# Performance work log

Hardware: AMD Instinct MI355X
Metric: run time of the kernel (lower is better)

The kernel has to match this reference:

```python
import jax, jax.numpy as jnp
import numpy as np
from math import factorial

LS = (0, 1, 2)
N_NODES = 30000
N_EDGES = 480000
E_CH = 2
C_IN = 4


def _cg_coeff(j1, m1, j2, m2, j, m):
    if m != m1 + m2 or j < abs(j1 - j2) or j > j1 + j2:
        return 0.0
    f = factorial
    pre = ((2 * j + 1) * f(j + j1 - j2) * f(j - j1 + j2) * f(j1 + j2 - j) / f(j1 + j2 + j + 1)) ** 0.5
    pre *= (f(j + m) * f(j - m) * f(j1 - m1) * f(j1 + m1) * f(j2 - m2) * f(j2 + m2)) ** 0.5
    s = 0.0
    for k in range(0, j1 + j2 - j + 1):
        d = [k, j1 + j2 - j - k, j1 - m1 - k, j2 + m2 - k, j - j2 + m1 + k, j - j1 - m2 + k]
        if any(v < 0 for v in d):
            continue
        s += (-1) ** k / np.prod([float(f(v)) for v in d])
    return pre * s


def _cg_matrix(l1, l2, l):
    # [2l+1, 2l1+1, 2l2+1]
    M = np.zeros((2 * l + 1, 2 * l1 + 1, 2 * l2 + 1), dtype=np.float32)
    for m in range(-l, l + 1):
        for m1 in range(-l1, l1 + 1):
            for m2 in range(-l2, l2 + 1):
                M[m + l, m1 + l1, m2 + l2] = _cg_coeff(l1, m1, l2, m2, l, m)
    return jnp.asarray(M)

CG_MATS = {}
for _l1 in LS:
    for _l2 in LS:
        for _lo in LS:
            if abs(_l1 - _l2) <= _lo <= _l1 + _l2:
                CG_MATS[(_l1, _l2, _lo)] = _cg_matrix(_l1, _l2, _lo)


def mp_layer(xs, edge_vals, src, dst, n_nodes):
    # gather src features, outer-product with edge channels, scatter-add to dst
    out = {}
    for l, x in xs.items():
        msg = x[src][:, None, :, :] * edge_vals[:, :, None, None]  # [E, Ech, C, 2l+1]
        msg = msg.reshape(msg.shape[0], -1, 2 * l + 1)
        out[l] = jax.ops.segment_sum(msg, dst, num_segments=n_nodes)
    return out


def cg_product(a, b):
    out = {}
    for lo in LS:
        chunks = []
        for l1 in LS:
            for l2 in LS:
                if abs(l1 - l2) <= lo <= l1 + l2:
                    C = CG_MATS[(l1, l2, lo)]
                    t = jnp.einsum('mpq,ncp,ndq->ncdm', C, a[l1], b[l2])
                    chunks.append(t.reshape(t.shape[0], -1, 2 * lo + 1))
        out[lo] = jnp.concatenate(chunks, axis=1)
    return out


def so3_linear(parts, weights):
    return {l: jnp.einsum('ncm,co->nom', parts[l], weights[l]) for l in parts}


def setup_inputs() -> dict:
    key = jax.random.key(0)
    ks = jax.random.split(key, 16)
    inp = {}
    for i, l in enumerate(LS):
        inp[f'x{l}'] = jax.random.normal(ks[i], (N_NODES, C_IN, 2 * l + 1), dtype=jnp.float32)
    inp['edge_vals'] = jax.random.normal(ks[3], (N_EDGES, E_CH), dtype=jnp.float32)
    w_shapes = {'W_xx0': (48, 8), 'W_xx1': (96, 8), 'W_xx2': (96, 8),
                'W_yx0': (96, 8), 'W_yx1': (192, 8), 'W_yx2': (192, 8),
                'W_yy0': (192, 8), 'W_yy1': (384, 8), 'W_yy2': (384, 8)}
    for i, (name, shp) in enumerate(w_shapes.items()):
        inp[name] = jax.random.normal(ks[4 + i], shp, dtype=jnp.float32) * 0.05
    inp['edge_idx'] = jax.random.randint(ks[13], (2, N_EDGES), 0, N_NODES, dtype=jnp.int64)
    return inp


def reference(x0, x1, x2, edge_vals,
              W_xx0, W_xx1, W_xx2,
              W_yx0, W_yx1, W_yx2,
              W_yy0, W_yy1, W_yy2,
              edge_idx):
    xs = {0: x0, 1: x1, 2: x2}
    src, dst = edge_idx[0], edge_idx[1]
    n = x0.shape[0]
    W_xx = {0: W_xx0, 1: W_xx1, 2: W_xx2}
    W_yx = {0: W_yx0, 1: W_yx1, 2: W_yx2}
    W_yy = {0: W_yy0, 1: W_yy1, 2: W_yy2}
    y = mp_layer(xs, edge_vals, src, dst, n)
    y_mp_mp = so3_linear(cg_product(y, y), W_yy)
    y_mp_id = so3_linear(cg_product(y, xs), W_yx)
    y_id_id = so3_linear(cg_product(xs, xs), W_xx)
    return tuple(y_mp_mp[l] + y_mp_id[l] + y_id_id[l] for l in LS)
```

## Files before the change

kernel.cpp:

```cpp
#include <hip/hip_runtime.h>
#include <stdint.h>

#define NN 30000
#define NE 480000
#define NB 469

constexpr double cfact(int n){ double r=1.0; for(int i=2;i<=n;i++) r*=(double)i; return r; }
constexpr double csqrt_(double x){ if(x<=0.0) return 0.0; double g = x<1.0?1.0:x; for(int i=0;i<200;i++) g = 0.5*(g + x/g); return g; }
constexpr double cg_coeff(int j1,int m1,int j2,int m2,int j,int m){
  if(m != m1+m2) return 0.0;
  int dj = j1-j2; if(dj<0) dj=-dj;
  if(j < dj || j > j1+j2) return 0.0;
  double pre = csqrt_((2*j+1)*cfact(j+j1-j2)*cfact(j-j1+j2)*cfact(j1+j2-j)/cfact(j1+j2+j+1));
  pre = pre * csqrt_(cfact(j+m)*cfact(j-m)*cfact(j1-m1)*cfact(j1+m1)*cfact(j2-m2)*cfact(j2+m2));
  double s = 0.0;
  for(int k=0;k<=j1+j2-j;k++){
    int d0=k, d1=j1+j2-j-k, d2=j1-m1-k, d3=j2+m2-k, d4=j-j2+m1+k, d5=j-j1-m2+k;
    if(d0<0||d1<0||d2<0||d3<0||d4<0||d5<0) continue;
    double term = 1.0/(cfact(d0)*cfact(d1)*cfact(d2)*cfact(d3)*cfact(d4)*cfact(d5));
    s += (k&1) ? -term : term;
  }
  return pre*s;
}

template<int L1,int L2,int LO> struct CGTab { float v[2*LO+1][2*L1+1][2*L2+1]; };

template<int L1,int L2,int LO>
constexpr CGTab<L1,L2,LO> make_cg(){
  CGTab<L1,L2,LO> t{};
  for(int m=-LO;m<=LO;m++)
    for(int p=-L1;p<=L1;p++)
      for(int q=-L2;q<=L2;q++)
        t.v[m+LO][p+L1][q+L2] = (float)cg_coeff(L1,p,L2,q,LO,m);
  return t;
}
template<int L1,int L2,int LO>
constexpr CGTab<L1,L2,LO> CG_TAB = make_cg<L1,L2,LO>();

template<int L1,int L2,int LO>
__device__ __forceinline__ void build_T(const float* av, const float* bv, float* T){
  constexpr int MA=2*L1+1, MB=2*L2+1, MO=2*LO+1;
  #pragma unroll
  for(int m=0;m<MO;m++) T[m]=0.f;
  #pragma unroll
  for(int m=0;m<MO;m++)
    #pragma unroll
    for(int p=0;p<MA;p++)
      #pragma unroll
      for(int q=0;q<MB;q++){
        const float cg = CG_TAB<L1,L2,LO>.v[m][p][q];
        if(cg!=0.0f) T[m]=fmaf(cg*av[p],bv[q],T[m]);
      }
}

template<int L1,int L2,int LO,int CA,int CB>
__device__ __forceinline__ void do_chunk(const float* __restrict__ A,
                                         const float* __restrict__ B,
                                         const float* __restrict__ W, int wb,
                                         float acc[8][2*LO+1])
{
  constexpr int MA=2*L1+1, MB=2*L2+1, MO=2*LO+1;
  float bv[CB][MB];
  #pragma unroll
  for(int d=0;d<CB;d++)
    #pragma unroll
    for(int q=0;q<MB;q++) bv[d][q] = B[(d*MB+q)*64];
  #pragma unroll 1
  for(int c=0;c<CA;c++){
    float av[MA];
    #pragma unroll
    for(int p=0;p<MA;p++) av[p] = A[(c*MA+p)*64];
    #pragma unroll
    for(int d=0;d<CB;d++){
      float T[MO];
      build_T<L1,L2,LO>(av, bv[d], T);
      const float* wr = W + (wb + c*CB + d)*8;
      #pragma unroll
      for(int o=0;o<8;o++){
        float w = wr[o];
        #pragma unroll
        for(int m=0;m<MO;m++) acc[o][m] = fmaf(w, T[m], acc[o][m]);
      }
    }
  }
}

template<int L1,int L2,int LO,int C,int SGN>
__device__ __forceinline__ void do_chunk_fold(const float* __restrict__ A1,
    const float* __restrict__ A2, const float* __restrict__ W, int wb1, int wb2,
    float acc[8][2*LO+1])
{
  constexpr int MA=2*L1+1, MB=2*L2+1, MO=2*LO+1;
  float bv[C][MB];
  #pragma unroll
  for(int d=0;d<C;d++)
    #pragma unroll
    for(int q=0;q<MB;q++) bv[d][q] = A2[(d*MB+q)*64];
  #pragma unroll 1
  for(int c=0;c<C;c++){
    float av[MA];
    #pragma unroll
    for(int p=0;p<MA;p++) av[p] = A1[(c*MA+p)*64];
    #pragma unroll
    for(int d=0;d<C;d++){
      float T[MO];
      build_T<L1,L2,LO>(av, bv[d], T);
      const float* w1 = W + (wb1 + c*C + d)*8;
      const float* w2 = W + (wb2 + d*C + c)*8;
      #pragma unroll
      for(int o=0;o<8;o++){
        float wf = (SGN>0) ? (w1[o] + w2[o]) : (w1[o] - w2[o]);
        #pragma unroll
        for(int m=0;m<MO;m++) acc[o][m] = fmaf(wf, T[m], acc[o][m]);
      }
    }
  }
}

template<int L,int LO,int C,int SGN>
__device__ __forceinline__ void do_chunk_tri(const float* __restrict__ Al,
    const float* __restrict__ W, int wb, float acc[8][2*LO+1])
{
  constexpr int M=2*L+1, MO=2*LO+1;
  float bv[C][M];
  #pragma unroll
  for(int d=0;d<C;d++)
    #pragma unroll
    for(int q=0;q<M;q++) bv[d][q] = Al[(d*M+q)*64];
  #pragma unroll 1
  for(int c=0;c<C-1;c++){
    float av[M];
    #pragma unroll
    for(int p=0;p<M;p++) av[p] = Al[(c*M+p)*64];
    #pragma unroll
    for(int d=0;d<C;d++){
      if(d > c){
        float T[MO];
        build_T<L,L,LO>(av, bv[d], T);
        const float* w1 = W + (wb + c*C + d)*8;
        const float* w2 = W + (wb + d*C + c)*8;
        #pragma unroll
        for(int o=0;o<8;o++){
          float wf = (SGN>0) ? (w1[o] + w2[o]) : (w1[o] - w2[o]);
          #pragma unroll
          for(int m=0;m<MO;m++) acc[o][m] = fmaf(wf, T[m], acc[o][m]);
        }
      }
    }
  }
}

template<int L,int LO,int C>
__device__ __forceinline__ void do_chunk_diagO(const float* __restrict__ Al,
    const float* __restrict__ W, int wb, float acc[8][2*LO+1])
{
  constexpr int M=2*L+1, MO=2*LO+1;
  #pragma unroll 1
  for(int c=0;c<C;c++){
    float av[M];
    #pragma unroll
    for(int p=0;p<M;p++) av[p] = Al[(c*M+p)*64];
    float T[MO];
    build_T<L,L,LO>(av, av, T);
    const float* wr = W + (wb + c*C + c)*8;
    #pragma unroll
    for(int o=0;o<8;o++){
      float w = wr[o];
      #pragma unroll
      for(int m=0;m<MO;m++) acc[o][m] = fmaf(w, T[m], acc[o][m]);
    }
  }
}

template<int LO,int CA,int CB>
__device__ __forceinline__ void run_chunks(
    const float* a0,const float* a1,const float* a2,
    const float* b0,const float* b1,const float* b2,
    const float* __restrict__ W, float acc[8][2*LO+1])
{
  constexpr int S = CA*CB;
  if constexpr (LO==0){
    do_chunk<0,0,0,CA,CB>(a0,b0,W,0*S,acc);
    do_chunk<1,1,0,CA,CB>(a1,b1,W,1*S,acc);
    do_chunk<2,2,0,CA,CB>(a2,b2,W,2*S,acc);
  } else if constexpr (LO==1){
    do_chunk<0,1,1,CA,CB>(a0,b1,W,0*S,acc);
    do_chunk<1,0,1,CA,CB>(a1,b0,W,1*S,acc);
    do_chunk<1,1,1,CA,CB>(a1,b1,W,2*S,acc);
    do_chunk<1,2,1,CA,CB>(a1,b2,W,3*S,acc);
    do_chunk<2,1,1,CA,CB>(a2,b1,W,4*S,acc);
    do_chunk<2,2,1,CA,CB>(a2,b2,W,5*S,acc);
  } else {
    do_chunk<0,2,2,CA,CB>(a0,b2,W,0*S,acc);
    do_chunk<1,1,2,CA,CB>(a1,b1,W,1*S,acc);
    do_chunk<1,2,2,CA,CB>(a1,b2,W,2*S,acc);
    do_chunk<2,0,2,CA,CB>(a2,b0,W,3*S,acc);
    do_chunk<2,1,2,CA,CB>(a2,b1,W,4*S,acc);
    do_chunk<2,2,2,CA,CB>(a2,b2,W,5*S,acc);
  }
}

template<int LO,int C>
__device__ __forceinline__ void run_chunks_sym(
    const float* a0,const float* a1,const float* a2,
    const float* __restrict__ W, float acc[8][2*LO+1])
{
  constexpr int S = C*C;
  if constexpr (LO==0){
    do_chunk_tri<0,0,C,+1>(a0,W,0*S,acc);  do_chunk_diagO<0,0,C>(a0,W,0*S,acc);
    do_chunk_tri<1,0,C,+1>(a1,W,1*S,acc);  do_chunk_diagO<1,0,C>(a1,W,1*S,acc);
    do_chunk_tri<2,0,C,+1>(a2,W,2*S,acc);  do_chunk_diagO<2,0,C>(a2,W,2*S,acc);
  } else if constexpr (LO==1){
    do_chunk_fold<0,1,1,C,+1>(a0,a1,W,0*S,1*S,acc);
    do_chunk_tri <1,1,C,-1>(a1,W,2*S,acc);
    do_chunk_fold<1,2,1,C,+1>(a1,a2,W,3*S,4*S,acc);
    do_chunk_tri <2,1,C,-1>(a2,W,5*S,acc);
  } else {
    do_chunk_fold<0,2,2,C,+1>(a0,a2,W,0*S,3*S,acc);
    do_chunk_tri <1,2,C,+1>(a1,W,1*S,acc);  do_chunk_diagO<1,2,C>(a1,W,1*S,acc);
    do_chunk_fold<1,2,2,C,-1>(a1,a2,W,2*S,4*S,acc);
    do_chunk_tri <2,2,C,+1>(a2,W,5*S,acc);  do_chunk_diagO<2,2,C>(a2,W,5*S,acc);
  }
}

template<int PROD,int LO>
__device__ __forceinline__ void do_item_lds(int lane,
    const float* __restrict__ sx, const float* __restrict__ sy,
    const float* __restrict__ W, float* __restrict__ so)
{
  const float *y0 = sy + lane, *y1 = sy + 8*64 + lane, *y2 = sy + 32*64 + lane;
  const float *x0 = sx + lane, *x1 = sx + 4*64 + lane, *x2 = sx + 16*64 + lane;
  constexpr int MO = 2*LO+1;

  float acc[8][MO];
  #pragma unroll
  for(int o=0;o<8;o++)
    #pragma unroll
    for(int m=0;m<MO;m++) acc[o][m]=0.f;

  if constexpr (PROD==0)      run_chunks_sym<LO,8>(y0,y1,y2,W,acc);
  else if constexpr (PROD==2) run_chunks_sym<LO,4>(x0,x1,x2,W,acc);
  else                        run_chunks<LO,8,4>(y0,y1,y2,x0,x1,x2,W,acc);

  constexpr int OB = (LO==0)?0:((LO==1)?8:32);
  #pragma unroll
  for(int o=0;o<8;o++)
    #pragma unroll
    for(int m=0;m<MO;m++)
      atomicAdd(&so[(OB + o*MO + m)*65 + lane], acc[o][m]);
}

struct WPtrs {
  const float* xx[3];
  const float* yx[3];
  const float* yy[3];
};

__global__ __launch_bounds__(256,2) void fused_kernel(
    const float* __restrict__ x0, const float* __restrict__ x1, const float* __restrict__ x2,
    const float4* __restrict__ edges, const int* __restrict__ offs,
    WPtrs w, float* __restrict__ out)
{
  __shared__ float sy[72*64];
  __shared__ float sx[36*64];
  __shared__ float so[72*65];

  const int tid = threadIdx.x;
  const int node0 = blockIdx.x*64;

  #pragma unroll
  for(int i=tid;i<72*65;i+=256) so[i]=0.f;

  for(int i=tid;i<64*4;i+=256){
    int gi = node0*4 + i;
    sx[(i&3)*64 + (i>>2)] = (gi < NN*4) ? x0[gi] : 0.f;
  }
  for(int i=tid;i<64*12;i+=256){
    int gi = node0*12 + i;
    sx[(4 + i%12)*64 + i/12] = (gi < NN*12) ? x1[gi] : 0.f;
  }
  for(int i=tid;i<64*20;i+=256){
    int gi = node0*20 + i;
    sx[(16 + i%20)*64 + i/20] = (gi < NN*20) ? x2[gi] : 0.f;
  }

  {
    int ln = tid >> 2, c = tid & 3;
    int gn = node0 + ln;
    float a0[2]={0.f,0.f};
    float a1[2][3]={}, a2[2][5]={};
    if(gn < NN){
      int k0 = offs[gn], k1 = offs[gn+1];
      for(int k=k0;k<k1;k++){
        float4 ed = edges[k];
        int src = __float_as_int(ed.x);
        float e0 = ed.y, e1 = ed.z;
        float v0 = x0[src*4 + c];
        const float* q1 = x1 + src*12 + c*3;
        const float* q2 = x2 + src*20 + c*5;
        a0[0] = fmaf(e0, v0, a0[0]);
        a0[1] = fmaf(e1, v0, a0[1]);
        #pragma unroll
        for(int m=0;m<3;m++){ float v=q1[m]; a1[0][m]=fmaf(e0,v,a1[0][m]); a1[1][m]=fmaf(e1,v,a1[1][m]); }
        #pragma unroll
        for(int m=0;m<5;m++){ float v=q2[m]; a2[0][m]=fmaf(e0,v,a2[0][m]); a2[1][m]=fmaf(e1,v,a2[1][m]); }
      }
    }
    #pragma unroll
    for(int ech=0;ech<2;ech++){
      int ch = ech*4 + c;
      sy[ch*64 + ln] = a0[ech];
      #pragma unroll
      for(int m=0;m<3;m++) sy[(8  + ch*3 + m)*64 + ln] = a1[ech][m];
      #pragma unroll
      for(int m=0;m<5;m++) sy[(32 + ch*5 + m)*64 + ln] = a2[ech][m];
    }
  }
  __syncthreads();

  {
    int lane = tid & 63, slot = tid >> 6;
    switch(slot){
      case 0: do_item_lds<1,2>(lane,sx,sy,w.yx[2],so); break;
      case 1: do_item_lds<0,2>(lane,sx,sy,w.yy[2],so); break;
      case 2: do_item_lds<0,1>(lane,sx,sy,w.yy[1],so);
              do_item_lds<2,2>(lane,sx,sy,w.xx[2],so);
              do_item_lds<0,0>(lane,sx,sy,w.yy[0],so); break;
      case 3: do_item_lds<1,1>(lane,sx,sy,w.yx[1],so);
              do_item_lds<2,1>(lane,sx,sy,w.xx[1],so);
              do_item_lds<1,0>(lane,sx,sy,w.yx[0],so);
              do_item_lds<2,0>(lane,sx,sy,w.xx[0],so); break;
    }
  }
  __syncthreads();

  for(int i=tid;i<64*8;i+=256){
    int n=i>>3, o=i&7;
    if(node0+n < NN) out[(node0+n)*8 + o] = so[o*65 + n];
  }
  for(int i=tid;i<64*24;i+=256){
    int n=i/24, r=i-n*24;
    if(node0+n < NN) out[NN*8 + (node0+n)*24 + r] = so[(8+r)*65 + n];
  }
  for(int i=tid;i<64*40;i+=256){
    int n=i/40, r=i-n*40;
    if(node0+n < NN) out[NN*32 + (node0+n)*40 + r] = so[(32+r)*65 + n];
  }
}

__global__ __launch_bounds__(256) void hist_kernel(const int* __restrict__ idx, int* __restrict__ cnt)
{
  int e = blockIdx.x*256 + threadIdx.x;
  if(e >= NE) return;
  atomicAdd(&cnt[idx[NE + e]], 1);
}

__global__ __launch_bounds__(256) void scan1_kernel(const int* __restrict__ cnt,
    int* __restrict__ offs, int* __restrict__ bt)
{
  __shared__ int wsum[4], wexc[4];
  int b = blockIdx.x, tid = threadIdx.x;
  int lane = tid & 63, wid = tid >> 6;
  int i0 = b*512 + tid*2;
  int v0 = (i0   < NN) ? cnt[i0]   : 0;
  int v1 = (i0+1 < NN) ? cnt[i0+1] : 0;
  int v = v0+v1, s = v;
  #pragma unroll
  for(int o=1;o<64;o<<=1){ int t=__shfl_up(s,o,64); if(lane>=o) s+=t; }
  if(lane==63) wsum[wid]=s;
  __syncthreads();
  if(tid<4){
    int wv=wsum[tid], x=wv;
    #pragma unroll
    for(int o=1;o<4;o<<=1){ int t=__shfl_up(x,o,4); if(tid>=o) x+=t; }
    wexc[tid]=x-wv;
    if(tid==3) bt[b]=x;
  }
  __syncthreads();
  int excl = s - v + wexc[wid];
  if(i0   < NN) offs[i0]   = excl;
  if(i0+1 < NN) offs[i0+1] = excl + v0;
}

__global__ __launch_bounds__(64) void scan2_kernel(int* __restrict__ bt,
    int* __restrict__ bte, int* __restrict__ offs)
{
  int tid = threadIdx.x;
  int v = bt[tid], s = v;
  #pragma unroll
  for(int o=1;o<64;o<<=1){ int t=__shfl_up(s,o,64); if(tid>=o) s+=t; }
  bte[tid] = s - v;
  if(tid==63) offs[NN] = s;
}

__global__ __launch_bounds__(512) void scan3_kernel(int* __restrict__ offs,
    const int* __restrict__ bte, int* __restrict__ cur)
{
  int i = blockIdx.x*512 + threadIdx.x;
  if(i >= NN) return;
  int o = offs[i] + bte[blockIdx.x];
  offs[i] = o;
  cur[i]  = o;
}

__global__ __launch_bounds__(256) void scatter_kernel(const int* __restrict__ idx,
    const float* __restrict__ ev, int* __restrict__ cur, float4* __restrict__ edges)
{
  int e = blockIdx.x*256 + threadIdx.x;
  if(e >= NE) return;
  int dst = idx[NE + e];
  int pos = atomicAdd(&cur[dst], 1);
  float4 r;
  r.x = __int_as_float(idx[e]);
  r.y = ev[2*e];
  r.z = ev[2*e+1];
  r.w = 0.f;
  edges[pos] = r;
}

extern "C" void kernel_launch(void* const* d_in, const int* in_sizes, int n_in,
                              void* d_out, int out_size, void* d_ws, size_t ws_size,
                              hipStream_t stream)
{
  const float* x0 = (const float*)d_in[0];
  const float* x1 = (const float*)d_in[1];
  const float* x2 = (const float*)d_in[2];
  const float* ev = (const float*)d_in[3];
  const int* idx  = (const int*)d_in[13];

  WPtrs w;
  for(int l=0;l<3;l++){
    w.xx[l] = (const float*)d_in[4+l];
    w.yx[l] = (const float*)d_in[7+l];
    w.yy[l] = (const float*)d_in[10+l];
  }

  float4* edges = (float4*)d_ws;
  int*    cnt   = (int*)(edges + NE);
  int*    offs  = cnt + NN;
  int*    cur   = offs + NN + 1;
  int*    bt    = cur + NN;
  int*    bte   = bt + 64;

  hipMemsetAsync(cnt, 0, (size_t)NN*sizeof(int), stream);

  hist_kernel<<<(NE+255)/256, 256, 0, stream>>>(idx, cnt);
  scan1_kernel<<<64, 256, 0, stream>>>(cnt, offs, bt);
  scan2_kernel<<<1, 64, 0, stream>>>(bt, bte, offs);
  scan3_kernel<<<64, 512, 0, stream>>>(offs, bte, cur);
  scatter_kernel<<<(NE+255)/256, 256, 0, stream>>>(idx, ev, cur, edges);

  fused_kernel<<<NB, 256, 0, stream>>>(x0, x1, x2, edges, offs, w, (float*)d_out);
}
```

Before: 246.0 us.

## Merge CSR build and fused compute into one persistent kernel with grid barriers

Replaces the memset plus five preprocessing launches (histogram, three-pass scan, scatter) and the fused compute kernel with a single kernel of 469 blocks. The stages are separated by software grid barriers built on atomic counters. The scan is reorganised so each block handles its own 64 nodes, and block 0 scans the block totals. This removes launch gaps and per-kernel tail effects. The risk is that all blocks must be co-resident for the barriers not to deadlock, and the spin-waiting with fewer threads in the atomic phases may cost throughput.

```diff
diff --git a/kernel.cpp b/kernel.cpp
--- a/kernel.cpp
+++ b/kernel.cpp
@@ -3,7 +3,7 @@
 
 #define NN 30000
 #define NE 480000
-#define NB 469
+#define NBLK 469
 
 constexpr double cfact(int n){ double r=1.0; for(int i=2;i<=n;i++) r*=(double)i; return r; }
 constexpr double csqrt_(double x){ if(x<=0.0) return 0.0; double g = x<1.0?1.0:x; for(int i=0;i<200;i++) g = 0.5*(g + x/g); return g; }
@@ -223,50 +223,135 @@
   }
 }
 
-template<int PROD,int LO>
-__device__ __forceinline__ void do_item_lds(int lane,
-    const float* __restrict__ sx, const float* __restrict__ sy,
-    const float* __restrict__ W, float* __restrict__ so)
-{
-  const float *y0 = sy + lane, *y1 = sy + 8*64 + lane, *y2 = sy + 32*64 + lane;
-  const float *x0 = sx + lane, *x1 = sx + 4*64 + lane, *x2 = sx + 16*64 + lane;
-  constexpr int MO = 2*LO+1;
-
-  float acc[8][MO];
-  #pragma unroll
-  for(int o=0;o<8;o++)
-    #pragma unroll
-    for(int m=0;m<MO;m++) acc[o][m]=0.f;
-
-  if constexpr (PROD==0)      run_chunks_sym<LO,8>(y0,y1,y2,W,acc);
-  else if constexpr (PROD==2) run_chunks_sym<LO,4>(x0,x1,x2,W,acc);
-  else                        run_chunks<LO,8,4>(y0,y1,y2,x0,x1,x2,W,acc);
-
-  constexpr int OB = (LO==0)?0:((LO==1)?8:32);
-  #pragma unroll
-  for(int o=0;o<8;o++)
-    #pragma unroll
-    for(int m=0;m<MO;m++)
-      atomicAdd(&so[(OB + o*MO + m)*65 + lane], acc[o][m]);
-}
-
 struct WPtrs {
   const float* xx[3];
   const float* yx[3];
   const float* yy[3];
 };
 
-__global__ __launch_bounds__(256,2) void fused_kernel(
+template<int PROD,int LO>
+__device__ __forceinline__ void do_item_lds(int lane,
+    const float* __restrict__ sx, const float* __restrict__ sy,
+    const WPtrs& w, float* __restrict__ so)
+{
+  const float *y0 = sy + lane, *y1 = sy + 8*64 + lane, *y2 = sy + 32*64 + lane;
+  const float *x0 = sx + lane, *x1 = sx + 4*64 + lane, *x2 = sx + 16*64 + lane;
+  constexpr int MO = 2*LO+1;
+  const float* W = (PROD==0) ? w.yy[LO] : ((PROD==1) ? w.yx[LO] : w.xx[LO]);
+
+  float acc[8][MO];
+  #pragma unroll
+  for(int o=0;o<8;o++)
+    #pragma unroll
+    for(int m=0;m<MO;m++) acc[o][m]=0.f;
+
+  if constexpr (PROD==0)      run_chunks_sym<LO,8>(y0,y1,y2,W,acc);
+  else if constexpr (PROD==2) run_chunks_sym<LO,4>(x0,x1,x2,W,acc);
+  else                        run_chunks<LO,8,4>(y0,y1,y2,x0,x1,x2,W,acc);
+
+  constexpr int OB = (LO==0)?0:((LO==1)?8:32);
+  #pragma unroll
+  for(int o=0;o<8;o++)
+    #pragma unroll
+    for(int m=0;m<MO;m++)
+      atomicAdd(&so[(OB + o*MO + m)*65 + lane], acc[o][m]);
+}
+
+__device__ __forceinline__ void gbar(int* __restrict__ ctr, int tid)
+{
+  __syncthreads();
+  if(tid==0){
+    __threadfence();
+    __hip_atomic_fetch_add(ctr, 1, __ATOMIC_ACQ_REL, __HIP_MEMORY_SCOPE_AGENT);
+    while(__hip_atomic_load(ctr, __ATOMIC_ACQUIRE, __HIP_MEMORY_SCOPE_AGENT) != NBLK)
+      __builtin_amdgcn_s_sleep(2);
+    __threadfence();
+  }
+  __syncthreads();
+}
+
+__global__ __launch_bounds__(256,2) void mega_kernel(
     const float* __restrict__ x0, const float* __restrict__ x1, const float* __restrict__ x2,
-    const float4* __restrict__ edges, const int* __restrict__ offs,
-    WPtrs w, float* __restrict__ out)
+    const float* __restrict__ ev, const int* __restrict__ idx, WPtrs w,
+    int* __restrict__ cnt, int* __restrict__ offs, int* __restrict__ cur,
+    int* __restrict__ bt, int* __restrict__ bte, float4* __restrict__ edges,
+    int* __restrict__ ctrs, float* __restrict__ out)
 {
   __shared__ float sy[72*64];
   __shared__ float sx[36*64];
   __shared__ float so[72*65];
 
   const int tid = threadIdx.x;
-  const int node0 = blockIdx.x*64;
+  const int b   = blockIdx.x;
+  const int gt  = b*256 + tid;
+  const int lane = tid & 63;
+  int* si = (int*)so;
+
+  for(int i=gt;i<NN;i+=NBLK*256) cnt[i]=0;
+  gbar(ctrs+0*16, tid);
+
+  for(int e=gt;e<NE;e+=NBLK*256) atomicAdd(&cnt[idx[NE+e]], 1);
+  gbar(ctrs+1*16, tid);
+
+  if(tid < 64){
+    int node = b*64 + tid;
+    int v = (node<NN) ? cnt[node] : 0;
+    int s = v;
+    #pragma unroll
+    for(int o=1;o<64;o<<=1){ int t=__shfl_up(s,o,64); if(lane>=o) s+=t; }
+    si[64+tid] = s - v;
+    if(tid==63) bt[b] = s;
+  }
+  gbar(ctrs+2*16, tid);
+
+  if(b == 0){
+    int i0 = 2*tid, i1 = 2*tid+1;
+    int v0 = (i0<NBLK) ? bt[i0] : 0;
+    int v1 = (i1<NBLK) ? bt[i1] : 0;
+    int s = v0+v1, incl = s;
+    #pragma unroll
+    for(int o=1;o<64;o<<=1){ int t=__shfl_up(incl,o,64); if(lane>=o) incl+=t; }
+    int wid = tid >> 6;
+    if(lane==63) si[8+wid] = incl;
+    __syncthreads();
+    if(tid < 4){
+      int wv = si[8+tid], x = wv;
+      #pragma unroll
+      for(int o=1;o<4;o<<=1){ int t=__shfl_up(x,o,4); if(tid>=o) x+=t; }
+      si[12+tid] = x - wv;
+    }
+    __syncthreads();
+    incl += si[12+wid];
+    int excl = incl - s;
+    if(i0<NBLK) bte[i0] = excl;
+    if(i1<NBLK) bte[i1] = excl + v0;
+    if(tid==255) offs[NN] = incl;
+  }
+  gbar(ctrs+3*16, tid);
+
+  if(tid < 64){
+    int node = b*64 + tid;
+    if(node < NN){
+      int o = si[64+tid] + bte[b];
+      offs[node] = o;
+      cur[node]  = o;
+    }
+  }
+  gbar(ctrs+4*16, tid);
+
+  for(int e=gt;e<NE;e+=NBLK*256){
+    int dst = idx[NE+e];
+    int pos = atomicAdd(&cur[dst], 1);
+    float4 r;
+    r.x = __int_as_float(idx[e]);
+    r.y = ev[2*e];
+    r.z = ev[2*e+1];
+    r.w = 0.f;
+    edges[pos] = r;
+  }
+  gbar(ctrs+5*16, tid);
+
+  const int node0 = b*64;
 
   #pragma unroll
   for(int i=tid;i<72*65;i+=256) so[i]=0.f;
@@ -319,17 +404,17 @@
   __syncthreads();
 
   {
-    int lane = tid & 63, slot = tid >> 6;
+    int slot = tid >> 6;
     switch(slot){
-      case 0: do_item_lds<1,2>(lane,sx,sy,w.yx[2],so); break;
-      case 1: do_item_lds<0,2>(lane,sx,sy,w.yy[2],so); break;
-      case 2: do_item_lds<0,1>(lane,sx,sy,w.yy[1],so);
-              do_item_lds<2,2>(lane,sx,sy,w.xx[2],so);
-              do_item_lds<0,0>(lane,sx,sy,w.yy[0],so); break;
-      case 3: do_item_lds<1,1>(lane,sx,sy,w.yx[1],so);
-              do_item_lds<2,1>(lane,sx,sy,w.xx[1],so);
-              do_item_lds<1,0>(lane,sx,sy,w.yx[0],so);
-              do_item_lds<2,0>(lane,sx,sy,w.xx[0],so); break;
+      case 0: do_item_lds<1,2>(lane,sx,sy,w,so); break;
+      case 1: do_item_lds<0,2>(lane,sx,sy,w,so); break;
+      case 2: do_item_lds<0,1>(lane,sx,sy,w,so);
+              do_item_lds<2,2>(lane,sx,sy,w,so);
+              do_item_lds<0,0>(lane,sx,sy,w,so); break;
+      case 3: do_item_lds<1,1>(lane,sx,sy,w,so);
+              do_item_lds<2,1>(lane,sx,sy,w,so);
+              do_item_lds<1,0>(lane,sx,sy,w,so);
+              do_item_lds<2,0>(lane,sx,sy,w,so); break;
     }
   }
   __syncthreads();
@@ -346,76 +431,6 @@
     int n=i/40, r=i-n*40;
     if(node0+n < NN) out[NN*32 + (node0+n)*40 + r] = so[(32+r)*65 + n];
   }
-}
-
-__global__ __launch_bounds__(256) void hist_kernel(const int* __restrict__ idx, int* __restrict__ cnt)
-{
-  int e = blockIdx.x*256 + threadIdx.x;
-  if(e >= NE) return;
-  atomicAdd(&cnt[idx[NE + e]], 1);
-}
-
-__global__ __launch_bounds__(256) void scan1_kernel(const int* __restrict__ cnt,
-    int* __restrict__ offs, int* __restrict__ bt)
-{
-  __shared__ int wsum[4], wexc[4];
-  int b = blockIdx.x, tid = threadIdx.x;
-  int lane = tid & 63, wid = tid >> 6;
-  int i0 = b*512 + tid*2;
-  int v0 = (i0   < NN) ? cnt[i0]   : 0;
-  int v1 = (i0+1 < NN) ? cnt[i0+1] : 0;
-  int v = v0+v1, s = v;
-  #pragma unroll
-  for(int o=1;o<64;o<<=1){ int t=__shfl_up(s,o,64); if(lane>=o) s+=t; }
-  if(lane==63) wsum[wid]=s;
-  __syncthreads();
-  if(tid<4){
-    int wv=wsum[tid], x=wv;
-    #pragma unroll
-    for(int o=1;o<4;o<<=1){ int t=__shfl_up(x,o,4); if(tid>=o) x+=t; }
-    wexc[tid]=x-wv;
-    if(tid==3) bt[b]=x;
-  }
-  __syncthreads();
-  int excl = s - v + wexc[wid];
-  if(i0   < NN) offs[i0]   = excl;
-  if(i0+1 < NN) offs[i0+1] = excl + v0;
-}
-
-__global__ __launch_bounds__(64) void scan2_kernel(int* __restrict__ bt,
-    int* __restrict__ bte, int* __restrict__ offs)
-{
-  int tid = threadIdx.x;
-  int v = bt[tid], s = v;
-  #pragma unroll
-  for(int o=1;o<64;o<<=1){ int t=__shfl_up(s,o,64); if(tid>=o) s+=t; }
-  bte[tid] = s - v;
-  if(tid==63) offs[NN] = s;
-}
-
-__global__ __launch_bounds__(512) void scan3_kernel(int* __restrict__ offs,
-    const int* __restrict__ bte, int* __restrict__ cur)
-{
-  int i = blockIdx.x*512 + threadIdx.x;
-  if(i >= NN) return;
-  int o = offs[i] + bte[blockIdx.x];
-  offs[i] = o;
-  cur[i]  = o;
-}
-
-__global__ __launch_bounds__(256) void scatter_kernel(const int* __restrict__ idx,
-    const float* __restrict__ ev, int* __restrict__ cur, float4* __restrict__ edges)
-{
-  int e = blockIdx.x*256 + threadIdx.x;
-  if(e >= NE) return;
-  int dst = idx[NE + e];
-  int pos = atomicAdd(&cur[dst], 1);
-  float4 r;
-  r.x = __int_as_float(idx[e]);
-  r.y = ev[2*e];
-  r.z = ev[2*e+1];
-  r.w = 0.f;
-  edges[pos] = r;
 }
 
 extern "C" void kernel_launch(void* const* d_in, const int* in_sizes, int n_in,
@@ -440,15 +455,12 @@
   int*    offs  = cnt + NN;
   int*    cur   = offs + NN + 1;
   int*    bt    = cur + NN;
-  int*    bte   = bt + 64;
-
-  hipMemsetAsync(cnt, 0, (size_t)NN*sizeof(int), stream);
-
-  hist_kernel<<<(NE+255)/256, 256, 0, stream>>>(idx, cnt);
-  scan1_kernel<<<64, 256, 0, stream>>>(cnt, offs, bt);
-  scan2_kernel<<<1, 64, 0, stream>>>(bt, bte, offs);
-  scan3_kernel<<<64, 512, 0, stream>>>(offs, bte, cur);
-  scatter_kernel<<<(NE+255)/256, 256, 0, stream>>>(idx, ev, cur, edges);
-
-  fused_kernel<<<NB, 256, 0, stream>>>(x0, x1, x2, edges, offs, w, (float*)d_out);
-}
+  int*    bte   = bt + NBLK;
+  int*    ctrs  = bte + NBLK;
+
+  hipMemsetAsync(ctrs, 0, 128*sizeof(int), stream);
+
+  mega_kernel<<<NBLK, 256, 0, stream>>>(x0, x1, x2, ev, idx, w,
+                                        cnt, offs, cur, bt, bte, edges, ctrs,
+                                        (float*)d_out);
+}
```

Result: slower. 517.9 us (+110.5%).
